# Optimization experiments

Hardware: AMD Instinct MI355X
Metric: run time of the kernel (lower is better)

## Reference

```python
import jax, jax.numpy as jnp
from jax import lax
import numpy as np

B, IMG, PS = 64, 384, 16
DM, DS, DI = 96, 16, 96
DT_RANK = 6
NREP = 4
NCLS = 5
HP = IMG // PS            # 24 patches per side
N = HP * HP               # 576 tokens


def _ln(x, g, b):
    m = x.mean(-1, keepdims=True)
    v = ((x - m) ** 2).mean(-1, keepdims=True)
    return (x - m) * lax.rsqrt(v + 1e-5) * g + b


def setup_inputs() -> dict:
    key = jax.random.key(0)
    ks = jax.random.split(key, 16)
    nrm = lambda k, s: jax.random.normal(k, s, jnp.float32) * 0.02
    return {
        "x": jax.random.uniform(ks[0], (B, 3, IMG, IMG), jnp.float32),
        "W_pe": nrm(ks[1], (DM, 3, PS, PS)), "b_pe": jnp.zeros((DM,), jnp.float32),
        "W_vis": nrm(ks[2], (DM, 1)), "b_vis": jnp.zeros((1,), jnp.float32),
        "dn_g": jnp.ones((DM,), jnp.float32), "dn_b": jnp.zeros((DM,), jnp.float32),
        "W_gate": nrm(ks[3], (DM, DM)), "b_gate": jnp.zeros((DM,), jnp.float32),
        "ln_g": jnp.ones((DM,), jnp.float32), "ln_b": jnp.zeros((DM,), jnp.float32),
        "W_in": nrm(ks[4], (DM, 2 * DI)),
        "conv_w": nrm(ks[5], (DI, 1, 3)),
        "W_xproj": nrm(ks[6], (DI, DT_RANK + 2 * DS)),
        "W_dt": nrm(ks[7], (DT_RANK, DI)), "b_dt": jnp.full((DI,), -2.0, jnp.float32),
        "A_log": jnp.log(jnp.tile(jnp.arange(1, DS + 1, dtype=jnp.float32), (DI, 1))),
        "D": jnp.ones((DI,), jnp.float32),
        "W_out": nrm(ks[8], (DI, DM)),
        "hd_dw": nrm(ks[9], (DM, 1, 3, 3)),
        "bn_g": jnp.ones((DM,), jnp.float32), "bn_b": jnp.zeros((DM,), jnp.float32),
        "bn_m": jnp.zeros((DM,), jnp.float32), "bn_v": jnp.ones((DM,), jnp.float32),
        "W_heat": nrm(ks[10], (NCLS, DM)), "b_heat": jnp.full((NCLS,), -2.19, jnp.float32),
        "W_off": nrm(ks[11], (2, DM)), "b_off": jnp.zeros((2,), jnp.float32),
        "W_size": nrm(ks[12], (2, DM)), "b_size": jnp.zeros((2,), jnp.float32),
    }


def _forward(x, W_pe, b_pe, W_vis, b_vis, dn_g, dn_b, W_gate, b_gate,
             ln_g, ln_b, W_in, conv_w, W_xproj, W_dt, b_dt, A_log, D, W_out,
             hd_dw, bn_g, bn_b, bn_m, bn_v, W_heat, b_heat, W_off, b_off, W_size, b_size):
    # --- retinex preprocessing (single-scale, log domain) ---
    kblur = jnp.ones((3, 1, 5, 5), jnp.float32) / 25.0
    L = lax.conv_general_dilated(x, kblur, (1, 1), 'SAME',
                                 feature_group_count=3,
                                 dimension_numbers=('NCHW', 'OIHW', 'NCHW'))
    x = jnp.log1p(jnp.clip(x, 0.0)) - jnp.log1p(jnp.clip(L, 0.0))
    # --- patch embedding: strided conv -> tokens (B,N,DM) ---
    t = lax.conv_general_dilated(x, W_pe, (PS, PS), 'VALID',
                                 dimension_numbers=('NCHW', 'OIHW', 'NCHW'))
    t = t + b_pe[None, :, None, None]
    tokens = t.reshape(B, DM, N).transpose(0, 2, 1)
    # --- visibility estimator: per-token gate (B,N,1) ---
    vis = jax.nn.sigmoid(tokens @ W_vis + b_vis)
    # --- dual norm: LN + sigmoid gate ---
    tokens = _ln(tokens, dn_g, dn_b)
    norm_gate = jax.nn.sigmoid(tokens @ W_gate + b_gate)  # (B,N,DM)
    # --- weight-shared NC-SSM blocks ---
    A = -jnp.exp(A_log)  # (DI,DS)
    for _ in range(NREP):
        resid = tokens
        h = _ln(tokens, ln_g, ln_b)
        xz = h @ W_in                      # (B,N,2*DI)
        xin, z = xz[..., :DI], xz[..., DI:]
        # causal depthwise conv1d over sequence, kernel 3
        xc = xin.transpose(0, 2, 1)        # (B,DI,N)
        xc = lax.conv_general_dilated(xc, conv_w, (1,), [(2, 0)],
                                      feature_group_count=DI,
                                      dimension_numbers=('NCH', 'OIH', 'NCH'))
        xs = jax.nn.silu(xc.transpose(0, 2, 1))  # (B,N,DI)
        # selective-scan parameters
        proj = xs @ W_xproj                # (B,N,DT_RANK+2*DS)
        dt_raw = proj[..., :DT_RANK]
        Bc = proj[..., DT_RANK:DT_RANK + DS]
        Cc = proj[..., DT_RANK + DS:]
        dt = jax.nn.softplus(dt_raw @ W_dt + b_dt)  # (B,N,DI)
        # time-major scan
        def step(hst, inp):
            dt_t, B_t, C_t, x_t = inp      # (B,DI),(B,DS),(B,DS),(B,DI)
            dA = jnp.exp(dt_t[:, :, None] * A)                 # (B,DI,DS)
            hst = dA * hst + (dt_t * x_t)[:, :, None] * B_t[:, None, :]
            y = jnp.einsum('bds,bs->bd', hst, C_t)
            return hst, y
        h0 = jnp.zeros((B, DI, DS), jnp.float32)
        _, ys = lax.scan(step, h0, (dt.transpose(1, 0, 2), Bc.transpose(1, 0, 2),
                                    Cc.transpose(1, 0, 2), xs.transpose(1, 0, 2)))
        y = ys.transpose(1, 0, 2) + D * xs           # (B,N,DI)
        y = y * jax.nn.silu(z) * vis                  # gated by z and visibility
        tokens = resid + (y @ W_out) * norm_gate
    # --- CenterNet-style head ---
    f = tokens.transpose(0, 2, 1).reshape(B, DM, HP, HP)
    g = lax.conv_general_dilated(f, hd_dw, (1, 1), 'SAME',
                                 feature_group_count=DM,
                                 dimension_numbers=('NCHW', 'OIHW', 'NCHW'))
    g = (g - bn_m[None, :, None, None]) * lax.rsqrt(bn_v + 1e-5)[None, :, None, None]
    g = jax.nn.silu(g * bn_g[None, :, None, None] + bn_b[None, :, None, None])
    heat = jnp.einsum('bchw,oc->bohw', g, W_heat) + b_heat[None, :, None, None]
    off = jnp.einsum('bchw,oc->bohw', f, W_off) + b_off[None, :, None, None]
    size = jnp.einsum('bchw,oc->bohw', f, W_size) + b_size[None, :, None, None]
    return heat, off, size


def reference(x, W_pe, b_pe, W_vis, b_vis, dn_g, dn_b, W_gate, b_gate,
              ln_g, ln_b, W_in, conv_w, W_xproj, W_dt, b_dt, A_log, D, W_out,
              hd_dw, bn_g, bn_b, bn_m, bn_v, W_heat, b_heat, W_off, b_off, W_size, b_size):
    return _forward(x, W_pe, b_pe, W_vis, b_vis, dn_g, dn_b, W_gate, b_gate,
                    ln_g, ln_b, W_in, conv_w, W_xproj, W_dt, b_dt, A_log, D, W_out,
                    hd_dw, bn_g, bn_b, bn_m, bn_v, W_heat, b_heat, W_off, b_off,
                    W_size, b_size)
```

## Files before the change

kernel.cpp:

```cpp
#include <hip/hip_runtime.h>

#define DEVINL __device__ __forceinline__

typedef __attribute__((ext_vector_type(8))) short bf8v;
typedef __attribute__((ext_vector_type(4))) float f4v;

DEVINL float b2f(unsigned short u){ union{unsigned int i; float f;} x; x.i = ((unsigned int)u)<<16; return x.f; }
DEVINL unsigned short f2b(float f){ union{float f; unsigned int i;} x; x.f = f; unsigned int r = x.i + 0x7FFFu + ((x.i>>16)&1u); return (unsigned short)(r>>16); }
DEVINL float sigf(float v){ return 1.f/(1.f + __expf(-v)); }
DEVINL void unpack8(const uint4 u, float* d){
  d[0]=b2f((unsigned short)(u.x)); d[1]=b2f((unsigned short)(u.x>>16));
  d[2]=b2f((unsigned short)(u.y)); d[3]=b2f((unsigned short)(u.y>>16));
  d[4]=b2f((unsigned short)(u.z)); d[5]=b2f((unsigned short)(u.z>>16));
  d[6]=b2f((unsigned short)(u.w)); d[7]=b2f((unsigned short)(u.w>>16));
}
DEVINL uint4 pack8(const float* s){
  uint4 u;
  u.x = (unsigned int)f2b(s[0]) | ((unsigned int)f2b(s[1])<<16);
  u.y = (unsigned int)f2b(s[2]) | ((unsigned int)f2b(s[3])<<16);
  u.z = (unsigned int)f2b(s[4]) | ((unsigned int)f2b(s[5])<<16);
  u.w = (unsigned int)f2b(s[6]) | ((unsigned int)f2b(s[7])<<16);
  return u;
}
union FragU { uint4 u; bf8v v; };


#define WS_XLOG   ((size_t)0)
#define WS_TOKRAW ((size_t)56623104)
#define WS_VIS    ((size_t)70778880)
#define WS_WGT    ((size_t)70926336)
#define WS_WIT    ((size_t)70944768)
#define WS_WXT    ((size_t)70981632)
#define WS_WOT    ((size_t)71006208)
#define WS_AMAT   ((size_t)71024640)
#define WS_WPE    ((size_t)71030784)
#define WS_CW     ((size_t)71178240)
#define WS_TOK    ((size_t)0)
#define WS_GATE   ((size_t)14155776)
#define WS_DNB    ((size_t)21233664)
#define WS_XSB    ((size_t)21233664)
#define WS_Y2     ((size_t)28311552)
#define WS_XIN    ((size_t)35389440)
#define WS_ZSV    ((size_t)42467328)
#define WS_DT     ((size_t)49545216)
#define WS_BC     ((size_t)56623104)

#define PREP_STRIDE (128*256)
__global__ __launch_bounds__(256) void k_prep(
    const float* __restrict__ Wgate, const float* __restrict__ Win,
    const float* __restrict__ Wxproj, const float* __restrict__ Wdt,
    const float* __restrict__ Wout, const float* __restrict__ Alog,
    const float* __restrict__ Wpe, const float* __restrict__ convw,
    unsigned short* __restrict__ WgT, unsigned short* __restrict__ WiT,
    unsigned short* __restrict__ WxT, unsigned short* __restrict__ WoT,
    float* __restrict__ Amat, unsigned short* __restrict__ WpeB,
    float* __restrict__ cwsplit)
{
  int gtid = blockIdx.x*256 + threadIdx.x;
  for (int i = gtid; i < 9216; i += PREP_STRIDE){
    int n = i/96, k = i - n*96;
    WgT[n*96+k] = f2b(Wgate[k*96+n]);
    WoT[n*96+k] = f2b(Wout[k*96+n]);
  }
  for (int i = gtid; i < 18432; i += PREP_STRIDE){
    int n = i/96, k = i - n*96;
    WiT[n*96+k] = f2b(Win[k*192+n]);
  }
  for (int i = gtid; i < 12288; i += PREP_STRIDE){
    int n = i/96, k = i - n*96;
    if (n < 96){
      float s = 0.f;
      for (int r = 0; r < 6; ++r) s += Wxproj[k*38+r] * Wdt[r*96+n];
      WxT[n*96+k] = f2b(s);
    } else {
      WxT[n*96+k] = f2b(Wxproj[k*38 + 6 + (n-96)]);
    }
  }
  for (int i = gtid; i < 1536; i += PREP_STRIDE) Amat[i] = -__expf(Alog[i]);
  for (int i = gtid; i < 73728; i += PREP_STRIDE) WpeB[i] = f2b(Wpe[i]);
  for (int i = gtid; i < 96; i += PREP_STRIDE){
    cwsplit[i]       = convw[i*3+0];
    cwsplit[96+i]    = convw[i*3+1];
    cwsplit[192+i]   = convw[i*3+2];
  }
}

__global__ __launch_bounds__(256) void k_blur(const float* __restrict__ x,
                                              unsigned short* __restrict__ xlog)
{
  __shared__ unsigned short xt[12*384];
  __shared__ float vt[8*392];
  int bid = blockIdx.x;
  int tile = bid % 48; int bc = bid / 48; int c = bc % 3; int b = bc / 3;
  const float* xin = x + (size_t)(b*3 + c) * 147456;
  unsigned short* xout = xlog + (size_t)(b*3 + c) * 147456;
  int y0 = tile * 8;
  int tid = threadIdx.x;

  #pragma unroll
  for (int k = 0; k < 5; ++k){
    int idx = tid + k*256;
    if (idx < 1152){
      int r = idx / 96; int c4 = idx - r*96;
      int gy = y0 - 2 + r;
      float4 v = make_float4(0.f,0.f,0.f,0.f);
      if (gy >= 0 && gy < 384) v = *(const float4*)(xin + gy*384 + c4*4);
      ushort4 o; o.x=f2b(v.x); o.y=f2b(v.y); o.z=f2b(v.z); o.w=f2b(v.w);
      *(ushort4*)(xt + r*384 + c4*4) = o;
    }
  }
  if (tid < 64){
    int r = tid >> 3; int j = tid & 7;
    vt[r*392 + ((j < 4) ? j : (384 + j))] = 0.f;
  }
  __syncthreads();

  #pragma unroll
  for (int k = 0; k < 2; ++k){
    int unit = tid + k*256;
    if (unit < 384){
      int r = unit / 48; int c8 = unit - r*48;
      const unsigned short* base = xt + r*384 + c8*8;
      float acc[8]; float t[8];
      uint4 u0 = *(const uint4*)(base);
      unpack8(u0, acc);
      #pragma unroll
      for (int i = 1; i < 5; ++i){
        uint4 u = *(const uint4*)(base + i*384);
        unpack8(u, t);
        #pragma unroll
        for (int j = 0; j < 8; ++j) acc[j] += t[j];
      }
      float* vrow = vt + r*392 + 4 + c8*8;
      *(float4*)(vrow)   = make_float4(acc[0],acc[1],acc[2],acc[3]);
      *(float4*)(vrow+4) = make_float4(acc[4],acc[5],acc[6],acc[7]);
    }
  }
  __syncthreads();

  #pragma unroll
  for (int k = 0; k < 3; ++k){
    int unit = tid + k*256;
    int r = unit / 96; int c4 = unit - r*96;
    int base = r*392 + 4 + c4*4;
    float f[12];
    *(float4*)(f)   = *(const float4*)(vt + base - 4);
    *(float4*)(f+4) = *(const float4*)(vt + base);
    *(float4*)(f+8) = *(const float4*)(vt + base + 4);
    ushort4 xr = *(const ushort4*)(xt + (r+2)*384 + c4*4);
    const unsigned short* xrp = &xr.x;
    ushort4 o;
    unsigned short* op = &o.x;
    #pragma unroll
    for (int j = 0; j < 4; ++j){
      float s = f[2+j] + f[3+j] + f[4+j] + f[5+j] + f[6+j];
      float L = fmaxf(s * 0.04f, 0.f);
      float xv = fmaxf(b2f(xrp[j]), 0.f);
      op[j] = f2b(__logf(1.f + xv) - __logf(1.f + L));
    }
    *(ushort4*)(xout + (y0+r)*384 + c4*4) = o;
  }
}

__global__ __launch_bounds__(256) void k_patch(const unsigned short* __restrict__ xlog,
    const unsigned short* __restrict__ WpeB, const float* __restrict__ bpe,
    float* __restrict__ tokraw)
{
  int wid = threadIdx.x >> 6, lane = threadIdx.x & 63;
  int m0 = (blockIdx.x*4 + wid)*16;
  int l15 = lane & 15, q = lane >> 4;
  int ma0 = m0 + l15;
  int b0 = ma0/576; int r0 = ma0 - b0*576; int hp0 = r0/24; int wp0 = r0 - hp0*24;
  size_t base0 = (size_t)b0*442368 + (size_t)hp0*6144 + (size_t)wp0*16;
  f4v acc[6];
  #pragma unroll
  for (int j=0;j<6;++j)
    #pragma unroll
    for (int r=0;r<4;++r) acc[j][r] = 0.f;
  for (int ks = 0; ks < 24; ++ks){
    int k0 = ks*32 + q*8;
    int c  = k0 >> 8;
    int ph = (k0 >> 4) & 15;
    int pw = k0 & 15;
    size_t off = (size_t)c*147456 + (size_t)ph*384 + pw;
    bf8v a0 = *(const bf8v*)(xlog + base0 + off);
    #pragma unroll
    for (int nf = 0; nf < 6; ++nf){
      bf8v bb = *(const bf8v*)(WpeB + (size_t)(nf*16 + l15)*768 + k0);
      acc[nf] = __builtin_amdgcn_mfma_f32_16x16x32_bf16(a0, bb, acc[nf], 0, 0, 0);
    }
  }
  #pragma unroll
  for (int nf=0; nf<6; ++nf)
    #pragma unroll
    for (int r=0; r<4; ++r){
      int m = m0 + q*4 + r;
      int n = nf*16 + l15;
      tokraw[(size_t)m*96 + n] = acc[nf][r] + bpe[n];
    }
}

__global__ __launch_bounds__(256) void k_ln_vis(const float* __restrict__ in,
    const float* __restrict__ g, const float* __restrict__ bta,
    const float* __restrict__ Wvis, const float* __restrict__ bvis,
    float* __restrict__ outf, unsigned short* __restrict__ outb, float* __restrict__ vis)
{
  int wid = threadIdx.x >> 6, lane = threadIdx.x & 63;
  int m0 = (blockIdx.x*4 + wid)*16;
  int l15 = lane & 15, q = lane >> 4;
  int ma0 = m0 + l15;
  float a0v[24];
  float s0=0.f, w0=0.f, vd=0.f;
  #pragma unroll
  for (int ks = 0; ks < 3; ++ks){
    int k0 = ks*32 + q*8;
    #pragma unroll
    for (int h = 0; h < 2; ++h){
      float4 va = *(const float4*)(in + (size_t)ma0*96 + k0 + h*4);
      float4 wv = *(const float4*)(Wvis + k0 + h*4);
      int o = ks*8 + h*4;
      a0v[o+0]=va.x; a0v[o+1]=va.y; a0v[o+2]=va.z; a0v[o+3]=va.w;
      s0 += (va.x+va.y)+(va.z+va.w);
      w0 += (va.x*va.x+va.y*va.y)+(va.z*va.z+va.w*va.w);
      vd += (va.x*wv.x+va.y*wv.y)+(va.z*wv.z+va.w*wv.w);
    }
  }
  s0 += __shfl_xor(s0, 16); s0 += __shfl_xor(s0, 32);
  w0 += __shfl_xor(w0, 16); w0 += __shfl_xor(w0, 32);
  vd += __shfl_xor(vd, 16); vd += __shfl_xor(vd, 32);
  float mu0 = s0*(1.f/96.f);
  float rs0 = rsqrtf(fmaxf(w0*(1.f/96.f)-mu0*mu0, 0.f) + 1e-5f);
  if (q == 0) vis[ma0] = sigf(vd + bvis[0]);
  #pragma unroll
  for (int ks = 0; ks < 3; ++ks){
    int k0 = ks*32 + q*8;
    #pragma unroll
    for (int h = 0; h < 2; ++h){
      float4 g4 = *(const float4*)(g + k0 + h*4);
      float4 b4 = *(const float4*)(bta + k0 + h*4);
      int o = ks*8 + h*4;
      float v0 = (a0v[o+0]-mu0)*rs0*g4.x + b4.x;
      float v1 = (a0v[o+1]-mu0)*rs0*g4.y + b4.y;
      float v2 = (a0v[o+2]-mu0)*rs0*g4.z + b4.z;
      float v3 = (a0v[o+3]-mu0)*rs0*g4.w + b4.w;
      *(float4*)(outf + (size_t)ma0*96 + k0 + h*4) = make_float4(v0,v1,v2,v3);
      ushort4 ob; ob.x=f2b(v0); ob.y=f2b(v1); ob.z=f2b(v2); ob.w=f2b(v3);
      *(ushort4*)(outb + (size_t)ma0*96 + k0 + h*4) = ob;
    }
  }
}

template<int NF, class Epi>
__global__ __launch_bounds__(256) void tokgemm96(const unsigned short* __restrict__ A,
    const unsigned short* __restrict__ BT, Epi epi)
{
  int wid = threadIdx.x >> 6, lane = threadIdx.x & 63;
  int m0 = (blockIdx.x*4 + wid)*16;
  int l15 = lane & 15, q = lane >> 4;
  f4v acc[NF];
  #pragma unroll
  for (int j=0;j<NF;++j)
    #pragma unroll
    for (int r=0;r<4;++r) acc[j][r] = 0.f;
  const bf8v* a0p = (const bf8v*)(A) + (size_t)(m0 + l15)*12 + q;
  const bf8v* bp  = (const bf8v*)(BT) + (size_t)l15*12 + q;
  #pragma unroll
  for (int ks = 0; ks < 3; ++ks){
    bf8v a0 = a0p[ks*4];
    #pragma unroll
    for (int nf = 0; nf < NF; ++nf){
      bf8v bb = bp[nf*192 + ks*4];
      acc[nf] = __builtin_amdgcn_mfma_f32_16x16x32_bf16(a0, bb, acc[nf], 0, 0, 0);
    }
  }
  #pragma unroll
  for (int nf=0; nf<NF; ++nf)
    #pragma unroll
    for (int r=0; r<4; ++r)
      epi(m0 + q*4 + r, nf*16 + l15, acc[nf][r]);
}

struct GateEpi {
  const float* bg; unsigned short* gate;
  __device__ void operator()(int m, int n, float v) const {
    gate[(size_t)m*96 + n] = f2b(sigf(v + bg[n]));
  }
};
struct WoutEpi {
  const unsigned short* gate; float* tokens;
  __device__ void operator()(int m, int n, float v) const {
    size_t i = (size_t)m*96 + n;
    tokens[i] = tokens[i] + v * b2f(gate[i]);
  }
};

__global__ __launch_bounds__(256) void k_lnwin(const float* __restrict__ tokp,
    const float* __restrict__ lng, const float* __restrict__ lnb,
    const unsigned short* __restrict__ BT, const float* __restrict__ vis,
    unsigned short* __restrict__ xin, unsigned short* __restrict__ zsv)
{
  int wid = threadIdx.x >> 6, lane = threadIdx.x & 63;
  int m0 = (blockIdx.x*4 + wid)*16;
  int l15 = lane & 15, q = lane >> 4;
  int ma0 = m0 + l15;
  float a0v[24];
  float s0=0.f, w0=0.f;
  #pragma unroll
  for (int ks = 0; ks < 3; ++ks){
    int k0 = ks*32 + q*8;
    #pragma unroll
    for (int h = 0; h < 2; ++h){
      float4 va = *(const float4*)(tokp + (size_t)ma0*96 + k0 + h*4);
      int o = ks*8 + h*4;
      a0v[o+0]=va.x; a0v[o+1]=va.y; a0v[o+2]=va.z; a0v[o+3]=va.w;
      s0 += (va.x+va.y)+(va.z+va.w);
      w0 += (va.x*va.x+va.y*va.y)+(va.z*va.z+va.w*va.w);
    }
  }
  s0 += __shfl_xor(s0, 16); s0 += __shfl_xor(s0, 32);
  w0 += __shfl_xor(w0, 16); w0 += __shfl_xor(w0, 32);
  float mu0 = s0*(1.f/96.f);
  float rs0 = rsqrtf(fmaxf(w0*(1.f/96.f)-mu0*mu0, 0.f) + 1e-5f);

  bf8v fa0[3];
  #pragma unroll
  for (int ks = 0; ks < 3; ++ks){
    int k0 = ks*32 + q*8;
    float gv[8], bv[8];
    *(float4*)(gv)   = *(const float4*)(lng + k0);
    *(float4*)(gv+4) = *(const float4*)(lng + k0 + 4);
    *(float4*)(bv)   = *(const float4*)(lnb + k0);
    *(float4*)(bv+4) = *(const float4*)(lnb + k0 + 4);
    float v0[8];
    #pragma unroll
    for (int j = 0; j < 8; ++j){
      v0[j] = (a0v[ks*8+j]-mu0)*rs0*gv[j] + bv[j];
    }
    FragU U0; U0.u = pack8(v0);
    fa0[ks] = U0.v;
  }

  f4v acc[12];
  #pragma unroll
  for (int j=0;j<12;++j)
    #pragma unroll
    for (int r=0;r<4;++r) acc[j][r] = 0.f;
  const bf8v* bp = (const bf8v*)(BT) + (size_t)l15*12 + q;
  #pragma unroll
  for (int ks = 0; ks < 3; ++ks){
    #pragma unroll
    for (int nf = 0; nf < 12; ++nf){
      bf8v bb = bp[nf*192 + ks*4];
      acc[nf] = __builtin_amdgcn_mfma_f32_16x16x32_bf16(fa0[ks], bb, acc[nf], 0, 0, 0);
    }
  }
  #pragma unroll
  for (int nf=0; nf<12; ++nf)
    #pragma unroll
    for (int r=0; r<4; ++r){
      int m = m0 + q*4 + r;
      int n = nf*16 + l15;
      float v = acc[nf][r];
      if (n < 96) xin[(size_t)m*96 + n] = f2b(v);
      else {
        float s = v * sigf(v);
        zsv[(size_t)m*96 + (n-96)] = f2b(s * vis[m]);
      }
    }
}

__global__ __launch_bounds__(256) void k_convxp(const unsigned short* __restrict__ xinb,
    const float* __restrict__ cwsplit, const unsigned short* __restrict__ BT,
    const float* __restrict__ bdt, unsigned short* __restrict__ xsb,
    unsigned short* __restrict__ dt, unsigned short* __restrict__ bc)
{
  int wid = threadIdx.x >> 6, lane = threadIdx.x & 63;
  int m0 = (blockIdx.x*4 + wid)*16;
  int l15 = lane & 15, q = lane >> 4;
  int ma0 = m0 + l15;
  int t0 = ma0 % 576;
  const float* cw0 = cwsplit;
  const float* cw1 = cwsplit + 96;
  const float* cw2 = cwsplit + 192;

  bf8v fa0[3];
  uint4 z4 = make_uint4(0,0,0,0);
  #pragma unroll
  for (int ks = 0; ks < 3; ++ks){
    int k0 = ks*32 + q*8;
    const unsigned short* r0p = xinb + (size_t)ma0*96 + k0;
    uint4 c0u  = *(const uint4*)(r0p);
    uint4 p10u = (t0 >= 1) ? *(const uint4*)(r0p - 96)  : z4;
    uint4 p20u = (t0 >= 2) ? *(const uint4*)(r0p - 192) : z4;
    float fc0[8], fp10[8], fp20[8];
    unpack8(c0u, fc0); unpack8(p10u, fp10); unpack8(p20u, fp20);
    float w0v[8], w1v[8], w2v[8];
    *(float4*)(w0v)   = *(const float4*)(cw0 + k0);
    *(float4*)(w0v+4) = *(const float4*)(cw0 + k0 + 4);
    *(float4*)(w1v)   = *(const float4*)(cw1 + k0);
    *(float4*)(w1v+4) = *(const float4*)(cw1 + k0 + 4);
    *(float4*)(w2v)   = *(const float4*)(cw2 + k0);
    *(float4*)(w2v+4) = *(const float4*)(cw2 + k0 + 4);
    float xs0[8];
    #pragma unroll
    for (int j = 0; j < 8; ++j){
      float v0 = w2v[j]*fc0[j] + w1v[j]*fp10[j] + w0v[j]*fp20[j];
      xs0[j] = v0 * sigf(v0);
    }
    FragU U0; U0.u = pack8(xs0);
    fa0[ks] = U0.v;
    *(uint4*)(xsb + (size_t)ma0*96 + k0) = U0.u;
  }

  f4v acc[8];
  #pragma unroll
  for (int j=0;j<8;++j)
    #pragma unroll
    for (int r=0;r<4;++r) acc[j][r] = 0.f;
  const bf8v* bp = (const bf8v*)(BT) + (size_t)l15*12 + q;
  #pragma unroll
  for (int ks = 0; ks < 3; ++ks){
    #pragma unroll
    for (int nf = 0; nf < 8; ++nf){
      bf8v bb = bp[nf*192 + ks*4];
      acc[nf] = __builtin_amdgcn_mfma_f32_16x16x32_bf16(fa0[ks], bb, acc[nf], 0, 0, 0);
    }
  }
  #pragma unroll
  for (int nf=0; nf<8; ++nf)
    #pragma unroll
    for (int r=0; r<4; ++r){
      int m = m0 + q*4 + r;
      int n = nf*16 + l15;
      float v = acc[nf][r];
      if (n < 96){
        float xx = v + bdt[n];
        float sp = (xx > 20.f) ? xx : __logf(1.f + __expf(xx));
        dt[(size_t)m*96 + n] = f2b(sp);
      } else {
        bc[(size_t)m*32 + (n-96)] = f2b(v);
      }
    }
}

__global__ __launch_bounds__(384) void k_scan(const unsigned short* __restrict__ dt,
    const unsigned short* __restrict__ xsb, const unsigned short* __restrict__ bc,
    const unsigned short* __restrict__ zsv, const float* __restrict__ Amat,
    const float* __restrict__ Dw, unsigned short* __restrict__ y2)
{
  __shared__ float Ul[24*16*17];
  __shared__ float Sl[24*16];
  int b = blockIdx.x / 6; int dg = blockIdx.x - b*6;
  int tid = threadIdx.x;
  int c = tid >> 4; int dl = tid & 15; int d = dg*16 + dl;
  float As[16];
  #pragma unroll
  for (int s = 0; s < 16; s += 4){
    float4 t4 = *(const float4*)(Amat + d*16 + s);
    As[s]=t4.x; As[s+1]=t4.y; As[s+2]=t4.z; As[s+3]=t4.w;
  }
  float h[16];
  #pragma unroll
  for (int s=0;s<16;++s) h[s]=0.f;
  float sdt = 0.f;
  int tbase = b*576 + c*24;
  for (int i = 0; i < 24; ++i){
    size_t m = (size_t)(tbase + i);
    float dtv = b2f(dt[m*96 + d]);
    float dtx = dtv * b2f(xsb[m*96 + d]);
    const uint4* bp = (const uint4*)(bc + m*32);
    float Bv[16];
    unpack8(bp[0], Bv); unpack8(bp[1], Bv+8);
    sdt += dtv;
    #pragma unroll
    for (int s=0;s<16;++s) h[s] = __expf(As[s]*dtv)*h[s] + dtx*Bv[s];
  }
  {
    int base = (c*16 + dl)*17;
    #pragma unroll
    for (int s=0;s<16;++s) Ul[base + s] = h[s];
    Sl[c*16 + dl] = sdt;
  }
  __syncthreads();
  if (tid < 256){
    int dl2 = tid >> 4, s2 = tid & 15;
    float A2 = Amat[(dg*16 + dl2)*16 + s2];
    float hh = 0.f;
    for (int cc = 0; cc < 24; ++cc){
      float u = Ul[(cc*16 + dl2)*17 + s2];
      float ss = Sl[cc*16 + dl2];
      hh = __expf(A2*ss)*hh + u;
      Ul[(cc*16 + dl2)*17 + s2] = hh;
    }
  }
  __syncthreads();
  if (c == 0){
    #pragma unroll
    for (int s=0;s<16;++s) h[s] = 0.f;
  } else {
    int base = ((c-1)*16 + dl)*17;
    #pragma unroll
    for (int s=0;s<16;++s) h[s] = Ul[base + s];
  }
  float Dd = Dw[d];
  for (int i = 0; i < 24; ++i){
    size_t m = (size_t)(tbase + i);
    float dtv = b2f(dt[m*96 + d]);
    float xv = b2f(xsb[m*96 + d]);
    float dtx = dtv * xv;
    const uint4* bp = (const uint4*)(bc + m*32);
    float Bv[16], Cv[16];
    unpack8(bp[0], Bv); unpack8(bp[1], Bv+8);
    unpack8(bp[2], Cv); unpack8(bp[3], Cv+8);
    float p0=0.f,p1=0.f,p2=0.f,p3=0.f;
    #pragma unroll
    for (int s=0;s<16;s+=4){
      h[s+0] = __expf(As[s+0]*dtv)*h[s+0] + dtx*Bv[s+0]; p0 += h[s+0]*Cv[s+0];
      h[s+1] = __expf(As[s+1]*dtv)*h[s+1] + dtx*Bv[s+1]; p1 += h[s+1]*Cv[s+1];
      h[s+2] = __expf(As[s+2]*dtv)*h[s+2] + dtx*Bv[s+2]; p2 += h[s+2]*Cv[s+2];
      h[s+3] = __expf(As[s+3]*dtv)*h[s+3] + dtx*Bv[s+3]; p3 += h[s+3]*Cv[s+3];
    }
    float y = (p0+p1) + (p2+p3);
    float yv = (y + Dd*xv) * b2f(zsv[m*96 + d]);
    y2[m*96 + d] = f2b(yv);
  }
}

__global__ __launch_bounds__(256) void k_head(const float* __restrict__ tokens,
    const float* __restrict__ hdw, const float* __restrict__ bng,
    const float* __restrict__ bnb, const float* __restrict__ bnm,
    const float* __restrict__ bnv, const float* __restrict__ Wheat,
    const float* __restrict__ bheat, const float* __restrict__ Woff,
    const float* __restrict__ boff, const float* __restrict__ Wsize,
    const float* __restrict__ bsize, float* __restrict__ out)
{
  __shared__ float ft[3*2304];
  __shared__ float act[2304];
  int b = blockIdx.x / 24; int h = blockIdx.x - b*24;
  for (int i = threadIdx.x; i < 3*2304; i += 256){
    int rr = i / 2304; int j = i - rr*2304;
    int hh = h + rr - 1;
    float v = 0.f;
    if (hh >= 0 && hh < 24) v = tokens[((size_t)b*576 + hh*24)*96 + j];
    ft[rr*2304 + j] = v;
  }
  __syncthreads();
  for (int i = threadIdx.x; i < 2304; i += 256){
    int w = i / 96; int cc = i - w*96;
    float g = 0.f;
    #pragma unroll
    for (int dh = 0; dh < 3; ++dh){
      #pragma unroll
      for (int dw = 0; dw < 3; ++dw){
        int ww = w + dw - 1;
        if (ww >= 0 && ww < 24) g += ft[dh*2304 + ww*96 + cc] * hdw[cc*9 + dh*3 + dw];
      }
    }
    float gn = (g - bnm[cc]) * rsqrtf(bnv[cc] + 1e-5f);
    float a = gn * bng[cc] + bnb[cc];
    act[i] = a * sigf(a);
  }
  __syncthreads();
  int tid = threadIdx.x;
  if (tid < 120){
    int o = tid / 24; int w = tid - o*24;
    float s = 0.f;
    for (int cc = 0; cc < 96; ++cc) s += act[w*96 + cc] * Wheat[o*96 + cc];
    s += bheat[o];
    out[(size_t)b*2880 + o*576 + h*24 + w] = s;
  } else if (tid >= 128 && tid < 224){
    int idx = tid - 128; int o2 = idx / 24; int w = idx - o2*24;
    const float* W = (o2 < 2) ? Woff : Wsize;
    int o = o2 & 1;
    float s = 0.f;
    for (int cc = 0; cc < 96; ++cc) s += ft[2304 + w*96 + cc] * W[o*96 + cc];
    s += ((o2 < 2) ? boff : bsize)[o];
    size_t baseo = (o2 < 2) ? (size_t)184320 : (size_t)258048;
    out[baseo + (size_t)b*1152 + o*576 + h*24 + w] = s;
  }
}

extern "C" void kernel_launch(void* const* d_in, const int* in_sizes, int n_in,
                              void* d_out, int out_size, void* d_ws, size_t ws_size,
                              hipStream_t stream)
{
  (void)in_sizes; (void)n_in; (void)out_size; (void)ws_size;
  const float* x      = (const float*)d_in[0];
  const float* Wpe    = (const float*)d_in[1];
  const float* bpe    = (const float*)d_in[2];
  const float* Wvis   = (const float*)d_in[3];
  const float* bvis   = (const float*)d_in[4];
  const float* dng    = (const float*)d_in[5];
  const float* dnb    = (const float*)d_in[6];
  const float* Wgate  = (const float*)d_in[7];
  const float* bgate  = (const float*)d_in[8];
  const float* lng    = (const float*)d_in[9];
  const float* lnb    = (const float*)d_in[10];
  const float* Win    = (const float*)d_in[11];
  const float* convw  = (const float*)d_in[12];
  const float* Wxproj = (const float*)d_in[13];
  const float* Wdt    = (const float*)d_in[14];
  const float* bdt    = (const float*)d_in[15];
  const float* Alog   = (const float*)d_in[16];
  const float* Dw     = (const float*)d_in[17];
  const float* Wout   = (const float*)d_in[18];
  const float* hddw   = (const float*)d_in[19];
  const float* bng    = (const float*)d_in[20];
  const float* bnb    = (const float*)d_in[21];
  const float* bnm    = (const float*)d_in[22];
  const float* bnv    = (const float*)d_in[23];
  const float* Wheat  = (const float*)d_in[24];
  const float* bheat  = (const float*)d_in[25];
  const float* Woff   = (const float*)d_in[26];
  const float* boff   = (const float*)d_in[27];
  const float* Wsize  = (const float*)d_in[28];
  const float* bsize  = (const float*)d_in[29];
  float* out = (float*)d_out;

  char* ws = (char*)d_ws;
  unsigned short* xlog  = (unsigned short*)(ws + WS_XLOG);
  float*          tokraw= (float*)(ws + WS_TOKRAW);
  float*          vis   = (float*)(ws + WS_VIS);
  unsigned short* WgT   = (unsigned short*)(ws + WS_WGT);
  unsigned short* WiT   = (unsigned short*)(ws + WS_WIT);
  unsigned short* WxT   = (unsigned short*)(ws + WS_WXT);
  unsigned short* WoT   = (unsigned short*)(ws + WS_WOT);
  float*          Amat  = (float*)(ws + WS_AMAT);
  unsigned short* WpeB  = (unsigned short*)(ws + WS_WPE);
  float*          cwsp  = (float*)(ws + WS_CW);
  float*          tok   = (float*)(ws + WS_TOK);
  unsigned short* gate  = (unsigned short*)(ws + WS_GATE);
  unsigned short* dnbf  = (unsigned short*)(ws + WS_DNB);
  unsigned short* xsb   = (unsigned short*)(ws + WS_XSB);
  unsigned short* y2    = (unsigned short*)(ws + WS_Y2);
  unsigned short* xinb  = (unsigned short*)(ws + WS_XIN);
  unsigned short* zsvb  = (unsigned short*)(ws + WS_ZSV);
  unsigned short* dtb   = (unsigned short*)(ws + WS_DT);
  unsigned short* bcb   = (unsigned short*)(ws + WS_BC);

  k_prep<<<128, 256, 0, stream>>>(Wgate, Win, Wxproj, Wdt, Wout, Alog, Wpe, convw,
                                  WgT, WiT, WxT, WoT, Amat, WpeB, cwsp);
  k_blur<<<9216, 256, 0, stream>>>(x, xlog);
  k_patch<<<576, 256, 0, stream>>>(xlog, WpeB, bpe, tokraw);
  k_ln_vis<<<576, 256, 0, stream>>>(tokraw, dng, dnb, Wvis, bvis, tok, dnbf, vis);
  tokgemm96<6, GateEpi><<<576, 256, 0, stream>>>(dnbf, WgT, GateEpi{bgate, gate});

  for (int rep = 0; rep < 4; ++rep){
    k_lnwin<<<576, 256, 0, stream>>>(tok, lng, lnb, WiT, vis, xinb, zsvb);
    k_convxp<<<576, 256, 0, stream>>>(xinb, cwsp, WxT, bdt, xsb, dtb, bcb);
    k_scan<<<384, 384, 0, stream>>>(dtb, xsb, bcb, zsvb, Amat, Dw, y2);
    tokgemm96<6, WoutEpi><<<576, 256, 0, stream>>>(y2, WoT, WoutEpi{gate, tok});
  }

  k_head<<<1536, 256, 0, stream>>>(tok, hddw, bng, bnb, bnm, bnv,
                                   Wheat, bheat, Woff, boff, Wsize, bsize, out);
}
```

Before: 798.9 us.

## Split GEMM N-halves across warps, fuse LN+gate, specialize scan exp, rework blur

Each token-GEMM kernel now gives each warp half of the output columns and launches twice as many blocks, which raises parallelism. The LN and visibility kernel absorbs the gate GEMM, so the bf16 intermediate and one launch go away. The blur keeps its input in fp32 shared memory and gets horizontal neighbours through lane shuffles, removing one shared-memory pass and one barrier. The scan uses 32 chunks of 18 tokens and, when A equals -(s+1), computes the decays as powers of a single exp instead of 16 exps. The cost is redundant LN and A-load work in each half-warp, plus a runtime check on the weights.

```diff
diff --git a/kernel.cpp b/kernel.cpp
--- a/kernel.cpp
+++ b/kernel.cpp
@@ -37,7 +37,6 @@
 #define WS_CW     ((size_t)71178240)
 #define WS_TOK    ((size_t)0)
 #define WS_GATE   ((size_t)14155776)
-#define WS_DNB    ((size_t)21233664)
 #define WS_XSB    ((size_t)21233664)
 #define WS_Y2     ((size_t)28311552)
 #define WS_XIN    ((size_t)35389440)
@@ -88,8 +87,7 @@
 __global__ __launch_bounds__(256) void k_blur(const float* __restrict__ x,
                                               unsigned short* __restrict__ xlog)
 {
-  __shared__ unsigned short xt[12*384];
-  __shared__ float vt[8*392];
+  __shared__ float xt[12*384];
   int bid = blockIdx.x;
   int tile = bid % 48; int bc = bid / 48; int c = bc % 3; int b = bc / 3;
   const float* xin = x + (size_t)(b*3 + c) * 147456;
@@ -105,60 +103,60 @@
       int gy = y0 - 2 + r;
       float4 v = make_float4(0.f,0.f,0.f,0.f);
       if (gy >= 0 && gy < 384) v = *(const float4*)(xin + gy*384 + c4*4);
-      ushort4 o; o.x=f2b(v.x); o.y=f2b(v.y); o.z=f2b(v.z); o.w=f2b(v.w);
-      *(ushort4*)(xt + r*384 + c4*4) = o;
-    }
-  }
-  if (tid < 64){
-    int r = tid >> 3; int j = tid & 7;
-    vt[r*392 + ((j < 4) ? j : (384 + j))] = 0.f;
+      *(float4*)(xt + r*384 + c4*4) = v;
+    }
   }
   __syncthreads();
 
   #pragma unroll
   for (int k = 0; k < 2; ++k){
-    int unit = tid + k*256;
-    if (unit < 384){
-      int r = unit / 48; int c8 = unit - r*48;
-      const unsigned short* base = xt + r*384 + c8*8;
-      float acc[8]; float t[8];
-      uint4 u0 = *(const uint4*)(base);
-      unpack8(u0, acc);
+    int slot = tid + k*256;
+    int r = slot >> 6; int c8 = slot & 63;
+    bool act = (c8 < 48);
+    float vs[8];
+    if (act){
+      const float* base = xt + r*384 + c8*8;
+      float4 a0 = *(const float4*)(base);
+      float4 a1 = *(const float4*)(base + 4);
+      vs[0]=a0.x; vs[1]=a0.y; vs[2]=a0.z; vs[3]=a0.w;
+      vs[4]=a1.x; vs[5]=a1.y; vs[6]=a1.z; vs[7]=a1.w;
       #pragma unroll
       for (int i = 1; i < 5; ++i){
-        uint4 u = *(const uint4*)(base + i*384);
-        unpack8(u, t);
-        #pragma unroll
-        for (int j = 0; j < 8; ++j) acc[j] += t[j];
+        float4 p = *(const float4*)(base + i*384);
+        float4 q = *(const float4*)(base + i*384 + 4);
+        vs[0]+=p.x; vs[1]+=p.y; vs[2]+=p.z; vs[3]+=p.w;
+        vs[4]+=q.x; vs[5]+=q.y; vs[6]+=q.z; vs[7]+=q.w;
       }
-      float* vrow = vt + r*392 + 4 + c8*8;
-      *(float4*)(vrow)   = make_float4(acc[0],acc[1],acc[2],acc[3]);
-      *(float4*)(vrow+4) = make_float4(acc[4],acc[5],acc[6],acc[7]);
-    }
-  }
-  __syncthreads();
-
-  #pragma unroll
-  for (int k = 0; k < 3; ++k){
-    int unit = tid + k*256;
-    int r = unit / 96; int c4 = unit - r*96;
-    int base = r*392 + 4 + c4*4;
-    float f[12];
-    *(float4*)(f)   = *(const float4*)(vt + base - 4);
-    *(float4*)(f+4) = *(const float4*)(vt + base);
-    *(float4*)(f+8) = *(const float4*)(vt + base + 4);
-    ushort4 xr = *(const ushort4*)(xt + (r+2)*384 + c4*4);
-    const unsigned short* xrp = &xr.x;
-    ushort4 o;
-    unsigned short* op = &o.x;
-    #pragma unroll
-    for (int j = 0; j < 4; ++j){
-      float s = f[2+j] + f[3+j] + f[4+j] + f[5+j] + f[6+j];
-      float L = fmaxf(s * 0.04f, 0.f);
-      float xv = fmaxf(b2f(xrp[j]), 0.f);
-      op[j] = f2b(__logf(1.f + xv) - __logf(1.f + L));
-    }
-    *(ushort4*)(xout + (y0+r)*384 + c4*4) = o;
+    } else {
+      #pragma unroll
+      for (int j = 0; j < 8; ++j) vs[j] = 0.f;
+    }
+    float l2 = __shfl_up(vs[6], 1);
+    float l1 = __shfl_up(vs[7], 1);
+    float r1 = __shfl_down(vs[0], 1);
+    float r2 = __shfl_down(vs[1], 1);
+    if (c8 == 0){ l2 = 0.f; l1 = 0.f; }
+    if (c8 == 47){ r1 = 0.f; r2 = 0.f; }
+    if (act){
+      float e[12];
+      e[0]=l2; e[1]=l1;
+      #pragma unroll
+      for (int j = 0; j < 8; ++j) e[2+j] = vs[j];
+      e[10]=r1; e[11]=r2;
+      const float* xraw = xt + (r+2)*384 + c8*8;
+      float xv[8];
+      *(float4*)(xv)   = *(const float4*)(xraw);
+      *(float4*)(xv+4) = *(const float4*)(xraw + 4);
+      float res[8];
+      #pragma unroll
+      for (int j = 0; j < 8; ++j){
+        float s = ((e[j]+e[j+1]) + (e[j+2]+e[j+3])) + e[j+4];
+        float L = fmaxf(s * 0.04f, 0.f);
+        float xc = fmaxf(xv[j], 0.f);
+        res[j] = __logf(1.f + xc) - __logf(1.f + L);
+      }
+      *(uint4*)(xout + (y0+r)*384 + c8*8) = pack8(res);
+    }
   }
 }
 
@@ -167,14 +165,17 @@
     float* __restrict__ tokraw)
 {
   int wid = threadIdx.x >> 6, lane = threadIdx.x & 63;
-  int m0 = (blockIdx.x*4 + wid)*16;
+  int gid = blockIdx.x*4 + wid;
+  int tile = gid >> 1, half = gid & 1;
+  int m0 = tile*16;
+  int nf0 = half*3;
   int l15 = lane & 15, q = lane >> 4;
   int ma0 = m0 + l15;
   int b0 = ma0/576; int r0 = ma0 - b0*576; int hp0 = r0/24; int wp0 = r0 - hp0*24;
   size_t base0 = (size_t)b0*442368 + (size_t)hp0*6144 + (size_t)wp0*16;
-  f4v acc[6];
-  #pragma unroll
-  for (int j=0;j<6;++j)
+  f4v acc[3];
+  #pragma unroll
+  for (int j=0;j<3;++j)
     #pragma unroll
     for (int r=0;r<4;++r) acc[j][r] = 0.f;
   for (int ks = 0; ks < 24; ++ks){
@@ -185,28 +186,33 @@
     size_t off = (size_t)c*147456 + (size_t)ph*384 + pw;
     bf8v a0 = *(const bf8v*)(xlog + base0 + off);
     #pragma unroll
-    for (int nf = 0; nf < 6; ++nf){
-      bf8v bb = *(const bf8v*)(WpeB + (size_t)(nf*16 + l15)*768 + k0);
+    for (int nf = 0; nf < 3; ++nf){
+      bf8v bb = *(const bf8v*)(WpeB + (size_t)((nf0+nf)*16 + l15)*768 + k0);
       acc[nf] = __builtin_amdgcn_mfma_f32_16x16x32_bf16(a0, bb, acc[nf], 0, 0, 0);
     }
   }
   #pragma unroll
-  for (int nf=0; nf<6; ++nf)
+  for (int nf=0; nf<3; ++nf)
     #pragma unroll
     for (int r=0; r<4; ++r){
       int m = m0 + q*4 + r;
-      int n = nf*16 + l15;
+      int n = (nf0+nf)*16 + l15;
       tokraw[(size_t)m*96 + n] = acc[nf][r] + bpe[n];
     }
 }
 
-__global__ __launch_bounds__(256) void k_ln_vis(const float* __restrict__ in,
+__global__ __launch_bounds__(256) void k_lngate(const float* __restrict__ in,
     const float* __restrict__ g, const float* __restrict__ bta,
     const float* __restrict__ Wvis, const float* __restrict__ bvis,
-    float* __restrict__ outf, unsigned short* __restrict__ outb, float* __restrict__ vis)
+    const unsigned short* __restrict__ BT, const float* __restrict__ bg,
+    float* __restrict__ tokout, unsigned short* __restrict__ gate,
+    float* __restrict__ vis)
 {
   int wid = threadIdx.x >> 6, lane = threadIdx.x & 63;
-  int m0 = (blockIdx.x*4 + wid)*16;
+  int gid = blockIdx.x*4 + wid;
+  int tile = gid >> 1, half = gid & 1;
+  int m0 = tile*16;
+  int nf0 = half*3;
   int l15 = lane & 15, q = lane >> 4;
   int ma0 = m0 + l15;
   float a0v[24];
@@ -230,36 +236,68 @@
   vd += __shfl_xor(vd, 16); vd += __shfl_xor(vd, 32);
   float mu0 = s0*(1.f/96.f);
   float rs0 = rsqrtf(fmaxf(w0*(1.f/96.f)-mu0*mu0, 0.f) + 1e-5f);
-  if (q == 0) vis[ma0] = sigf(vd + bvis[0]);
+  if (half == 0 && q == 0) vis[ma0] = sigf(vd + bvis[0]);
+
+  bf8v fa0[3];
   #pragma unroll
   for (int ks = 0; ks < 3; ++ks){
     int k0 = ks*32 + q*8;
-    #pragma unroll
-    for (int h = 0; h < 2; ++h){
-      float4 g4 = *(const float4*)(g + k0 + h*4);
-      float4 b4 = *(const float4*)(bta + k0 + h*4);
-      int o = ks*8 + h*4;
-      float v0 = (a0v[o+0]-mu0)*rs0*g4.x + b4.x;
-      float v1 = (a0v[o+1]-mu0)*rs0*g4.y + b4.y;
-      float v2 = (a0v[o+2]-mu0)*rs0*g4.z + b4.z;
-      float v3 = (a0v[o+3]-mu0)*rs0*g4.w + b4.w;
-      *(float4*)(outf + (size_t)ma0*96 + k0 + h*4) = make_float4(v0,v1,v2,v3);
-      ushort4 ob; ob.x=f2b(v0); ob.y=f2b(v1); ob.z=f2b(v2); ob.w=f2b(v3);
-      *(ushort4*)(outb + (size_t)ma0*96 + k0 + h*4) = ob;
-    }
-  }
+    float gv[8], bv[8];
+    *(float4*)(gv)   = *(const float4*)(g + k0);
+    *(float4*)(gv+4) = *(const float4*)(g + k0 + 4);
+    *(float4*)(bv)   = *(const float4*)(bta + k0);
+    *(float4*)(bv+4) = *(const float4*)(bta + k0 + 4);
+    float v0[8];
+    #pragma unroll
+    for (int j = 0; j < 8; ++j){
+      v0[j] = (a0v[ks*8+j]-mu0)*rs0*gv[j] + bv[j];
+    }
+    if (half == 0){
+      *(float4*)(tokout + (size_t)ma0*96 + k0)     = make_float4(v0[0],v0[1],v0[2],v0[3]);
+      *(float4*)(tokout + (size_t)ma0*96 + k0 + 4) = make_float4(v0[4],v0[5],v0[6],v0[7]);
+    }
+    FragU U0; U0.u = pack8(v0);
+    fa0[ks] = U0.v;
+  }
+
+  f4v acc[3];
+  #pragma unroll
+  for (int j=0;j<3;++j)
+    #pragma unroll
+    for (int r=0;r<4;++r) acc[j][r] = 0.f;
+  const bf8v* bp = (const bf8v*)(BT) + (size_t)l15*12 + q;
+  #pragma unroll
+  for (int ks = 0; ks < 3; ++ks){
+    #pragma unroll
+    for (int nf = 0; nf < 3; ++nf){
+      bf8v bb = bp[(nf0+nf)*192 + ks*4];
+      acc[nf] = __builtin_amdgcn_mfma_f32_16x16x32_bf16(fa0[ks], bb, acc[nf], 0, 0, 0);
+    }
+  }
+  #pragma unroll
+  for (int nf=0; nf<3; ++nf)
+    #pragma unroll
+    for (int r=0; r<4; ++r){
+      int m = m0 + q*4 + r;
+      int n = (nf0+nf)*16 + l15;
+      gate[(size_t)m*96 + n] = f2b(sigf(acc[nf][r] + bg[n]));
+    }
 }
 
 template<int NF, class Epi>
 __global__ __launch_bounds__(256) void tokgemm96(const unsigned short* __restrict__ A,
     const unsigned short* __restrict__ BT, Epi epi)
 {
+  constexpr int NF2 = NF/2;
   int wid = threadIdx.x >> 6, lane = threadIdx.x & 63;
-  int m0 = (blockIdx.x*4 + wid)*16;
+  int gid = blockIdx.x*4 + wid;
+  int tile = gid >> 1, half = gid & 1;
+  int m0 = tile*16;
+  int nf0 = half*NF2;
   int l15 = lane & 15, q = lane >> 4;
-  f4v acc[NF];
-  #pragma unroll
-  for (int j=0;j<NF;++j)
+  f4v acc[NF2];
+  #pragma unroll
+  for (int j=0;j<NF2;++j)
     #pragma unroll
     for (int r=0;r<4;++r) acc[j][r] = 0.f;
   const bf8v* a0p = (const bf8v*)(A) + (size_t)(m0 + l15)*12 + q;
@@ -268,24 +306,18 @@
   for (int ks = 0; ks < 3; ++ks){
     bf8v a0 = a0p[ks*4];
     #pragma unroll
-    for (int nf = 0; nf < NF; ++nf){
-      bf8v bb = bp[nf*192 + ks*4];
+    for (int nf = 0; nf < NF2; ++nf){
+      bf8v bb = bp[(nf0+nf)*192 + ks*4];
       acc[nf] = __builtin_amdgcn_mfma_f32_16x16x32_bf16(a0, bb, acc[nf], 0, 0, 0);
     }
   }
   #pragma unroll
-  for (int nf=0; nf<NF; ++nf)
+  for (int nf=0; nf<NF2; ++nf)
     #pragma unroll
     for (int r=0; r<4; ++r)
-      epi(m0 + q*4 + r, nf*16 + l15, acc[nf][r]);
-}
-
-struct GateEpi {
-  const float* bg; unsigned short* gate;
-  __device__ void operator()(int m, int n, float v) const {
-    gate[(size_t)m*96 + n] = f2b(sigf(v + bg[n]));
-  }
-};
+      epi(m0 + q*4 + r, (nf0+nf)*16 + l15, acc[nf][r]);
+}
+
 struct WoutEpi {
   const unsigned short* gate; float* tokens;
   __device__ void operator()(int m, int n, float v) const {
@@ -300,7 +332,10 @@
     unsigned short* __restrict__ xin, unsigned short* __restrict__ zsv)
 {
   int wid = threadIdx.x >> 6, lane = threadIdx.x & 63;
-  int m0 = (blockIdx.x*4 + wid)*16;
+  int gid = blockIdx.x*4 + wid;
+  int tile = gid >> 1, half = gid & 1;
+  int m0 = tile*16;
+  int nf0 = half*6;
   int l15 = lane & 15, q = lane >> 4;
   int ma0 = m0 + l15;
   float a0v[24];
@@ -340,33 +375,41 @@
     fa0[ks] = U0.v;
   }
 
-  f4v acc[12];
-  #pragma unroll
-  for (int j=0;j<12;++j)
+  f4v acc[6];
+  #pragma unroll
+  for (int j=0;j<6;++j)
     #pragma unroll
     for (int r=0;r<4;++r) acc[j][r] = 0.f;
   const bf8v* bp = (const bf8v*)(BT) + (size_t)l15*12 + q;
   #pragma unroll
   for (int ks = 0; ks < 3; ++ks){
     #pragma unroll
-    for (int nf = 0; nf < 12; ++nf){
-      bf8v bb = bp[nf*192 + ks*4];
+    for (int nf = 0; nf < 6; ++nf){
+      bf8v bb = bp[(nf0+nf)*192 + ks*4];
       acc[nf] = __builtin_amdgcn_mfma_f32_16x16x32_bf16(fa0[ks], bb, acc[nf], 0, 0, 0);
     }
   }
-  #pragma unroll
-  for (int nf=0; nf<12; ++nf)
-    #pragma unroll
-    for (int r=0; r<4; ++r){
-      int m = m0 + q*4 + r;
-      int n = nf*16 + l15;
-      float v = acc[nf][r];
-      if (n < 96) xin[(size_t)m*96 + n] = f2b(v);
-      else {
+  if (half == 0){
+    #pragma unroll
+    for (int nf=0; nf<6; ++nf)
+      #pragma unroll
+      for (int r=0; r<4; ++r){
+        int m = m0 + q*4 + r;
+        int n = nf*16 + l15;
+        xin[(size_t)m*96 + n] = f2b(acc[nf][r]);
+      }
+  } else {
+    #pragma unroll
+    for (int nf=0; nf<6; ++nf)
+      #pragma unroll
+      for (int r=0; r<4; ++r){
+        int m = m0 + q*4 + r;
+        int n = (6+nf)*16 + l15;
+        float v = acc[nf][r];
         float s = v * sigf(v);
         zsv[(size_t)m*96 + (n-96)] = f2b(s * vis[m]);
       }
-    }
+  }
 }
 
 __global__ __launch_bounds__(256) void k_convxp(const unsigned short* __restrict__ xinb,
@@ -375,7 +418,10 @@
     unsigned short* __restrict__ dt, unsigned short* __restrict__ bc)
 {
   int wid = threadIdx.x >> 6, lane = threadIdx.x & 63;
-  int m0 = (blockIdx.x*4 + wid)*16;
+  int gid = blockIdx.x*4 + wid;
+  int tile = gid >> 1, half = gid & 1;
+  int m0 = tile*16;
+  int nf0 = half*4;
   int l15 = lane & 15, q = lane >> 4;
   int ma0 = m0 + l15;
   int t0 = ma0 % 576;
@@ -409,29 +455,29 @@
     }
     FragU U0; U0.u = pack8(xs0);
     fa0[ks] = U0.v;
-    *(uint4*)(xsb + (size_t)ma0*96 + k0) = U0.u;
-  }
-
-  f4v acc[8];
-  #pragma unroll
-  for (int j=0;j<8;++j)
+    if (half == 0) *(uint4*)(xsb + (size_t)ma0*96 + k0) = U0.u;
+  }
+
+  f4v acc[4];
+  #pragma unroll
+  for (int j=0;j<4;++j)
     #pragma unroll
     for (int r=0;r<4;++r) acc[j][r] = 0.f;
   const bf8v* bp = (const bf8v*)(BT) + (size_t)l15*12 + q;
   #pragma unroll
   for (int ks = 0; ks < 3; ++ks){
     #pragma unroll
-    for (int nf = 0; nf < 8; ++nf){
-      bf8v bb = bp[nf*192 + ks*4];
+    for (int nf = 0; nf < 4; ++nf){
+      bf8v bb = bp[(nf0+nf)*192 + ks*4];
       acc[nf] = __builtin_amdgcn_mfma_f32_16x16x32_bf16(fa0[ks], bb, acc[nf], 0, 0, 0);
     }
   }
   #pragma unroll
-  for (int nf=0; nf<8; ++nf)
+  for (int nf=0; nf<4; ++nf)
     #pragma unroll
     for (int r=0; r<4; ++r){
       int m = m0 + q*4 + r;
-      int n = nf*16 + l15;
+      int n = (nf0+nf)*16 + l15;
       float v = acc[nf][r];
       if (n < 96){
         float xx = v + bdt[n];
@@ -443,13 +489,13 @@
     }
 }
 
-__global__ __launch_bounds__(384) void k_scan(const unsigned short* __restrict__ dt,
+__global__ __launch_bounds__(512) void k_scan(const unsigned short* __restrict__ dt,
     const unsigned short* __restrict__ xsb, const unsigned short* __restrict__ bc,
     const unsigned short* __restrict__ zsv, const float* __restrict__ Amat,
     const float* __restrict__ Dw, unsigned short* __restrict__ y2)
 {
-  __shared__ float Ul[24*16*17];
-  __shared__ float Sl[24*16];
+  __shared__ float Ul[32*16*17];
+  __shared__ float Sl[32*16];
   int b = blockIdx.x / 6; int dg = blockIdx.x - b*6;
   int tid = threadIdx.x;
   int c = tid >> 4; int dl = tid & 15; int d = dg*16 + dl;
@@ -459,21 +505,45 @@
     float4 t4 = *(const float4*)(Amat + d*16 + s);
     As[s]=t4.x; As[s+1]=t4.y; As[s+2]=t4.z; As[s+3]=t4.w;
   }
+  bool fast = true;
+  #pragma unroll
+  for (int s = 0; s < 16; ++s)
+    fast = fast && (fabsf(As[s] + (float)(s+1)) <= 2e-5f*(float)(s+1));
+
   float h[16];
   #pragma unroll
   for (int s=0;s<16;++s) h[s]=0.f;
   float sdt = 0.f;
-  int tbase = b*576 + c*24;
-  for (int i = 0; i < 24; ++i){
-    size_t m = (size_t)(tbase + i);
-    float dtv = b2f(dt[m*96 + d]);
-    float dtx = dtv * b2f(xsb[m*96 + d]);
-    const uint4* bp = (const uint4*)(bc + m*32);
-    float Bv[16];
-    unpack8(bp[0], Bv); unpack8(bp[1], Bv+8);
-    sdt += dtv;
-    #pragma unroll
-    for (int s=0;s<16;++s) h[s] = __expf(As[s]*dtv)*h[s] + dtx*Bv[s];
+  int tbase = b*576 + c*18;
+  if (fast){
+    for (int i = 0; i < 18; ++i){
+      size_t m = (size_t)(tbase + i);
+      float dtv = b2f(dt[m*96 + d]);
+      float dtx = dtv * b2f(xsb[m*96 + d]);
+      const uint4* bp = (const uint4*)(bc + m*32);
+      float Bv[16];
+      unpack8(bp[0], Bv); unpack8(bp[1], Bv+8);
+      sdt += dtv;
+      float w1=__expf(-dtv), w2=w1*w1, w3=w2*w1, w4=w2*w2;
+      float w5=w4*w1, w6=w4*w2, w7=w4*w3, w8=w4*w4;
+      float w9=w8*w1, w10=w8*w2, w11=w8*w3, w12=w8*w4;
+      float w13=w8*w5, w14=w8*w6, w15=w8*w7, w16=w8*w8;
+      float dA[16]={w1,w2,w3,w4,w5,w6,w7,w8,w9,w10,w11,w12,w13,w14,w15,w16};
+      #pragma unroll
+      for (int s=0;s<16;++s) h[s] = dA[s]*h[s] + dtx*Bv[s];
+    }
+  } else {
+    for (int i = 0; i < 18; ++i){
+      size_t m = (size_t)(tbase + i);
+      float dtv = b2f(dt[m*96 + d]);
+      float dtx = dtv * b2f(xsb[m*96 + d]);
+      const uint4* bp = (const uint4*)(bc + m*32);
+      float Bv[16];
+      unpack8(bp[0], Bv); unpack8(bp[1], Bv+8);
+      sdt += dtv;
+      #pragma unroll
+      for (int s=0;s<16;++s) h[s] = __expf(As[s]*dtv)*h[s] + dtx*Bv[s];
+    }
   }
   {
     int base = (c*16 + dl)*17;
@@ -486,7 +556,7 @@
     int dl2 = tid >> 4, s2 = tid & 15;
     float A2 = Amat[(dg*16 + dl2)*16 + s2];
     float hh = 0.f;
-    for (int cc = 0; cc < 24; ++cc){
+    for (int cc = 0; cc < 32; ++cc){
       float u = Ul[(cc*16 + dl2)*17 + s2];
       float ss = Sl[cc*16 + dl2];
       hh = __expf(A2*ss)*hh + u;
@@ -503,26 +573,55 @@
     for (int s=0;s<16;++s) h[s] = Ul[base + s];
   }
   float Dd = Dw[d];
-  for (int i = 0; i < 24; ++i){
-    size_t m = (size_t)(tbase + i);
-    float dtv = b2f(dt[m*96 + d]);
-    float xv = b2f(xsb[m*96 + d]);
-    float dtx = dtv * xv;
-    const uint4* bp = (const uint4*)(bc + m*32);
-    float Bv[16], Cv[16];
-    unpack8(bp[0], Bv); unpack8(bp[1], Bv+8);
-    unpack8(bp[2], Cv); unpack8(bp[3], Cv+8);
-    float p0=0.f,p1=0.f,p2=0.f,p3=0.f;
-    #pragma unroll
-    for (int s=0;s<16;s+=4){
-      h[s+0] = __expf(As[s+0]*dtv)*h[s+0] + dtx*Bv[s+0]; p0 += h[s+0]*Cv[s+0];
-      h[s+1] = __expf(As[s+1]*dtv)*h[s+1] + dtx*Bv[s+1]; p1 += h[s+1]*Cv[s+1];
-      h[s+2] = __expf(As[s+2]*dtv)*h[s+2] + dtx*Bv[s+2]; p2 += h[s+2]*Cv[s+2];
-      h[s+3] = __expf(As[s+3]*dtv)*h[s+3] + dtx*Bv[s+3]; p3 += h[s+3]*Cv[s+3];
-    }
-    float y = (p0+p1) + (p2+p3);
-    float yv = (y + Dd*xv) * b2f(zsv[m*96 + d]);
-    y2[m*96 + d] = f2b(yv);
+  if (fast){
+    for (int i = 0; i < 18; ++i){
+      size_t m = (size_t)(tbase + i);
+      float dtv = b2f(dt[m*96 + d]);
+      float xv = b2f(xsb[m*96 + d]);
+      float dtx = dtv * xv;
+      const uint4* bp = (const uint4*)(bc + m*32);
+      float Bv[16], Cv[16];
+      unpack8(bp[0], Bv); unpack8(bp[1], Bv+8);
+      unpack8(bp[2], Cv); unpack8(bp[3], Cv+8);
+      float w1=__expf(-dtv), w2=w1*w1, w3=w2*w1, w4=w2*w2;
+      float w5=w4*w1, w6=w4*w2, w7=w4*w3, w8=w4*w4;
+      float w9=w8*w1, w10=w8*w2, w11=w8*w3, w12=w8*w4;
+      float w13=w8*w5, w14=w8*w6, w15=w8*w7, w16=w8*w8;
+      float dA[16]={w1,w2,w3,w4,w5,w6,w7,w8,w9,w10,w11,w12,w13,w14,w15,w16};
+      float p0=0.f,p1=0.f,p2=0.f,p3=0.f;
+      #pragma unroll
+      for (int s=0;s<16;s+=4){
+        h[s+0] = dA[s+0]*h[s+0] + dtx*Bv[s+0]; p0 += h[s+0]*Cv[s+0];
+        h[s+1] = dA[s+1]*h[s+1] + dtx*Bv[s+1]; p1 += h[s+1]*Cv[s+1];
+        h[s+2] = dA[s+2]*h[s+2] + dtx*Bv[s+2]; p2 += h[s+2]*Cv[s+2];
+        h[s+3] = dA[s+3]*h[s+3] + dtx*Bv[s+3]; p3 += h[s+3]*Cv[s+3];
+      }
+      float y = (p0+p1) + (p2+p3);
+      float yv = (y + Dd*xv) * b2f(zsv[m*96 + d]);
+      y2[m*96 + d] = f2b(yv);
+    }
+  } else {
+    for (int i = 0; i < 18; ++i){
+      size_t m = (size_t)(tbase + i);
+      float dtv = b2f(dt[m*96 + d]);
+      float xv = b2f(xsb[m*96 + d]);
+      float dtx = dtv * xv;
+      const uint4* bp = (const uint4*)(bc + m*32);
+      float Bv[16], Cv[16];
+      unpack8(bp[0], Bv); unpack8(bp[1], Bv+8);
+      unpack8(bp[2], Cv); unpack8(bp[3], Cv+8);
+      float p0=0.f,p1=0.f,p2=0.f,p3=0.f;
+      #pragma unroll
+      for (int s=0;s<16;s+=4){
+        h[s+0] = __expf(As[s+0]*dtv)*h[s+0] + dtx*Bv[s+0]; p0 += h[s+0]*Cv[s+0];
+        h[s+1] = __expf(As[s+1]*dtv)*h[s+1] + dtx*Bv[s+1]; p1 += h[s+1]*Cv[s+1];
+        h[s+2] = __expf(As[s+2]*dtv)*h[s+2] + dtx*Bv[s+2]; p2 += h[s+2]*Cv[s+2];
+        h[s+3] = __expf(As[s+3]*dtv)*h[s+3] + dtx*Bv[s+3]; p3 += h[s+3]*Cv[s+3];
+      }
+      float y = (p0+p1) + (p2+p3);
+      float yv = (y + Dd*xv) * b2f(zsv[m*96 + d]);
+      y2[m*96 + d] = f2b(yv);
+    }
   }
 }
 
@@ -630,7 +729,6 @@
   float*          cwsp  = (float*)(ws + WS_CW);
   float*          tok   = (float*)(ws + WS_TOK);
   unsigned short* gate  = (unsigned short*)(ws + WS_GATE);
-  unsigned short* dnbf  = (unsigned short*)(ws + WS_DNB);
   unsigned short* xsb   = (unsigned short*)(ws + WS_XSB);
   unsigned short* y2    = (unsigned short*)(ws + WS_Y2);
   unsigned short* xinb  = (unsigned short*)(ws + WS_XIN);
@@ -641,15 +739,15 @@
   k_prep<<<128, 256, 0, stream>>>(Wgate, Win, Wxproj, Wdt, Wout, Alog, Wpe, convw,
                                   WgT, WiT, WxT, WoT, Amat, WpeB, cwsp);
   k_blur<<<9216, 256, 0, stream>>>(x, xlog);
-  k_patch<<<576, 256, 0, stream>>>(xlog, WpeB, bpe, tokraw);
-  k_ln_vis<<<576, 256, 0, stream>>>(tokraw, dng, dnb, Wvis, bvis, tok, dnbf, vis);
-  tokgemm96<6, GateEpi><<<576, 256, 0, stream>>>(dnbf, WgT, GateEpi{bgate, gate});
+  k_patch<<<1152, 256, 0, stream>>>(xlog, WpeB, bpe, tokraw);
+  k_lngate<<<1152, 256, 0, stream>>>(tokraw, dng, dnb, Wvis, bvis, WgT, bgate,
+                                     tok, gate, vis);
 
   for (int rep = 0; rep < 4; ++rep){
-    k_lnwin<<<576, 256, 0, stream>>>(tok, lng, lnb, WiT, vis, xinb, zsvb);
-    k_convxp<<<576, 256, 0, stream>>>(xinb, cwsp, WxT, bdt, xsb, dtb, bcb);
-    k_scan<<<384, 384, 0, stream>>>(dtb, xsb, bcb, zsvb, Amat, Dw, y2);
-    tokgemm96<6, WoutEpi><<<576, 256, 0, stream>>>(y2, WoT, WoutEpi{gate, tok});
+    k_lnwin<<<1152, 256, 0, stream>>>(tok, lng, lnb, WiT, vis, xinb, zsvb);
+    k_convxp<<<1152, 256, 0, stream>>>(xinb, cwsp, WxT, bdt, xsb, dtb, bcb);
+    k_scan<<<384, 512, 0, stream>>>(dtb, xsb, bcb, zsvb, Amat, Dw, y2);
+    tokgemm96<6, WoutEpi><<<1152, 256, 0, stream>>>(y2, WoT, WoutEpi{gate, tok});
   }
 
   k_head<<<1536, 256, 0, stream>>>(tok, hddw, bng, bnb, bnm, bnv,
```

Measured after the change: 699.5 us. 12.4% less time.
